# Kernel tuning notes

Measured on AMD Instinct MI355X. Metric: run time of the kernel, lower is better.

The kernel has to match this reference:

```python
import jax, jax.numpy as jnp
import numpy as np

EPS = 1e-5


def setup_inputs() -> dict:
    key = jax.random.key(0)
    ks = jax.random.split(key, 12)
    B, C, H, W = 1, 512, 64, 64
    d = C // 8
    inp = {
        "x": jax.random.normal(ks[0], (B, C, H, W), jnp.float32),
        "y": jax.random.normal(ks[1], (B, C, H, W), jnp.float32),
        "s_m": jax.random.uniform(ks[2], (H, W), jnp.float32),
        "q_m": jax.random.uniform(ks[3], (H, W), jnp.float32),
        "Wq": jax.random.normal(ks[4], (d, C), jnp.float32) * (1.0 / np.sqrt(C)),
        "bq": jnp.zeros((d,), jnp.float32),
        "Wk": jax.random.normal(ks[5], (d, C), jnp.float32) * (1.0 / np.sqrt(C)),
        "bk": jnp.zeros((d,), jnp.float32),
        "Wv": jax.random.normal(ks[6], (C, C), jnp.float32) * (1.0 / np.sqrt(C)),
        "bv": jnp.zeros((C,), jnp.float32),
        "W1": jax.random.normal(ks[7], (C, C), jnp.float32) * (1.0 / np.sqrt(C)),
        "b1": jnp.zeros((C,), jnp.float32),
        "W2": jax.random.normal(ks[8], (C, C), jnp.float32) * (1.0 / np.sqrt(C)),
        "b2": jnp.zeros((C,), jnp.float32),
        "gamma": jnp.ones((1, C, H, W), jnp.float32),
        "beta": jnp.zeros((1, C, H, W), jnp.float32),
    }
    return inp


def _conv1x1(x, Wt, b):
    # 1x1 Conv2d == per-pixel channel matmul
    return jnp.einsum("bchw,oc->bohw", x, Wt) + b[None, :, None, None]


def reference(x, y, s_m, q_m, Wq, bq, Wk, bk, Wv, bv, W1, b1, W2, b2, gamma, beta):
    B, C, H, W = x.shape
    N = H * W
    scale = (C // 8) ** (-0.5)

    q_m = jnp.where(q_m > 0.8, 1.0, 0.0).astype(x.dtype)
    x_fg = x * s_m[None, None]
    y_fg = y * q_m[None, None]

    def branch(q_in, k_in, v_in, use_max):
        q = _conv1x1(q_in, Wq, bq).reshape(B, -1, N).transpose(0, 2, 1) * scale  # [B,N,d]
        k = _conv1x1(k_in, Wk, bk).reshape(B, -1, N)                             # [B,d,N]
        v = _conv1x1(v_in, Wv, bv).reshape(B, -1, N)                             # [B,C,N]
        attn = jnp.einsum("bqd,bdk->bqk", q, k)                                  # [B,N,N]
        stat = jnp.max(attn) if use_max else jnp.min(attn)
        thr = (stat + jnp.mean(attn)) * 0.5
        attn = jnp.where(attn < thr, jnp.asarray(-999.0, attn.dtype), attn)
        attn = jax.nn.softmax(attn, axis=-1)
        out = jnp.einsum("bck,bqk->bcq", v, attn).reshape(B, C, H, W)
        h = out.transpose(0, 2, 3, 1)                                            # [B,H,W,C]
        h = jnp.maximum(h @ W1.T + b1, 0.0) @ W2.T + b2
        out = h.transpose(0, 3, 1, 2)
        # LayerNorm over all trailing dims [1,C,H,W] (B==1)
        mu = jnp.mean(out)
        var = jnp.mean((out - mu) ** 2)
        out = (out - mu) * jax.lax.rsqrt(var + EPS) * gamma + beta
        return out

    outx = branch(x_fg, y_fg, y_fg, True)
    outx = outx * s_m[None, None] + x * (1.0 - s_m)[None, None]
    outy = branch(y_fg, x, x, False)
    outy = outy * q_m[None, None] + y * (1.0 - q_m)[None, None]
    return outx, outy
```

## Files before the change

### kernel.cpp

```cpp
#include <hip/hip_runtime.h>
#include <math.h>

#define C_DIM 512
#define N_DIM 4096
#define CN (C_DIM * N_DIM)
#define SZO (N_DIM * C_DIM)
#define NN ((size_t)N_DIM * N_DIM)
#define NN_TOT ((long long)N_DIM * N_DIM)

typedef __attribute__((ext_vector_type(4))) float f32x4;
typedef __attribute__((ext_vector_type(8))) short short8;

__device__ __forceinline__ ushort f2bf(float f) {
    unsigned u = __float_as_uint(f);
    unsigned r = u + 0x7FFFu + ((u >> 16) & 1u);
    return (ushort)(r >> 16);
}
__device__ __forceinline__ float bf2f(ushort h) {
    return __uint_as_float((unsigned)h << 16);
}

__device__ __forceinline__ void gload16(const void* g, void* l) {
    __builtin_amdgcn_global_load_lds(
        (const __attribute__((address_space(1))) void*)g,
        (__attribute__((address_space(3))) void*)l, 16, 0, 0);
}

__global__ __launch_bounds__(256) void tconv64(
    const float* __restrict__ x, const float* __restrict__ y,
    ushort* __restrict__ xbT, ushort* __restrict__ ybT)
{
    const float* X = blockIdx.z ? y : x;
    ushort* XT = blockIdx.z ? ybT : xbT;
    __shared__ float t[64][65];
    const int c0 = blockIdx.x * 64;
    const int r0 = blockIdx.y * 64;
    const int ty = threadIdx.x >> 4, tx = threadIdx.x & 15;
    #pragma unroll
    for (int i = 0; i < 4; ++i) {
        int r = ty + i * 16;
        float4 v = *(const float4*)&X[(size_t)(r0 + r) * N_DIM + c0 + tx * 4];
        t[r][tx * 4 + 0] = v.x; t[r][tx * 4 + 1] = v.y;
        t[r][tx * 4 + 2] = v.z; t[r][tx * 4 + 3] = v.w;
    }
    __syncthreads();
    #pragma unroll
    for (int i = 0; i < 4; ++i) {
        int nn = ty + i * 16;
        ushort4 o;
        o.x = f2bf(t[tx * 4 + 0][nn]); o.y = f2bf(t[tx * 4 + 1][nn]);
        o.z = f2bf(t[tx * 4 + 2][nn]); o.w = f2bf(t[tx * 4 + 3][nn]);
        *(ushort4*)&XT[(size_t)(c0 + nn) * C_DIM + r0 + tx * 4] = o;
    }
}

__global__ __launch_bounds__(256) void cvtw3(
    const float* __restrict__ Wv, const float* __restrict__ W1,
    const float* __restrict__ W2, ushort* __restrict__ Wvb,
    ushort* __restrict__ W1b, ushort* __restrict__ W2b)
{
    const float* in  = (blockIdx.y == 0) ? Wv : (blockIdx.y == 1) ? W1 : W2;
    ushort*      out = (blockIdx.y == 0) ? Wvb : (blockIdx.y == 1) ? W1b : W2b;
    int i = (blockIdx.x * 256 + threadIdx.x) * 4;
    float4 v = *(const float4*)&in[i];
    ushort4 o = { f2bf(v.x), f2bf(v.y), f2bf(v.z), f2bf(v.w) };
    *(ushort4*)&out[i] = o;
}

template<int BM, int BN>
__global__ __launch_bounds__(256) void mfma_g(
    const ushort* __restrict__ A0, const ushort* __restrict__ A1,
    const ushort* __restrict__ B0, const ushort* __restrict__ B1,
    void* __restrict__ Out, size_t outBrStride,
    int M, int N, int K, int kLen, int nkz,
    const float* __restrict__ bias, int biasMode,
    const float* __restrict__ mask0, int mm0,
    const float* __restrict__ mask1, int mm1,
    int doRelu, int outBf16)
{
    constexpr int WAVES_M = BM / 64;
    constexpr int WAVES_N = 4 / WAVES_M;
    constexpr int WN = BN / WAVES_N;
    constexpr int FM = 4;
    constexpr int FN = WN / 16;
    constexpr int NCHUNK = (BM + BN) / 16;

    __shared__ ushort As[2][BM * 32];
    __shared__ ushort Bs[2][BN * 32];
    const int tid  = threadIdx.x;
    const int lane = tid & 63;
    const int wid  = tid >> 6;
    const int z  = blockIdx.z;
    const int br = z / nkz;
    const int kz = z % nkz;
    const ushort* A = br ? A1 : A0;
    const ushort* B = br ? B1 : B0;
    const float* mask = br ? mask1 : mask0;
    const int maskMode = br ? mm1 : mm0;

    const int m0 = blockIdx.y * BM, n0 = blockIdx.x * BN;
    const int wm = wid / WAVES_N, wn = wid % WAVES_N;
    const int wr = wm * 64, wc = wn * WN;
    const int kOff = kz * kLen;
    const int lrow = lane >> 2;
    const int lk   = (lane & 3) * 8;

    auto stage = [&](int buf, int t) {
        #pragma unroll
        for (int c = wid; c < NCHUNK; c += 4) {
            if (c < BM / 16) {
                gload16(A + (size_t)(m0 + c * 16 + lrow) * K + kOff + t * 32 + lk,
                        &As[buf][c * 512]);
            } else {
                int cb = c - BM / 16;
                gload16(B + (size_t)(n0 + cb * 16 + lrow) * K + kOff + t * 32 + lk,
                        &Bs[buf][cb * 512]);
            }
        }
    };

    f32x4 acc[FM][FN] = {};
    const int fr = lane & 15;
    const int k8 = (lane >> 4) * 8;
    const int nt = kLen / 32;

    stage(0, 0);
    asm volatile("s_waitcnt vmcnt(0)" ::: "memory");
    __syncthreads();
    int cur = 0;
    for (int t = 0; t < nt; ++t) {
        if (t + 1 < nt) stage(cur ^ 1, t + 1);
        short8 af[FM], bf[FN];
        #pragma unroll
        for (int mr = 0; mr < FM; ++mr)
            af[mr] = *(const short8*)&As[cur][(wr + mr * 16 + fr) * 32 + k8];
        #pragma unroll
        for (int nc = 0; nc < FN; ++nc)
            bf[nc] = *(const short8*)&Bs[cur][(wc + nc * 16 + fr) * 32 + k8];
        #pragma unroll
        for (int mr = 0; mr < FM; ++mr)
            #pragma unroll
            for (int nc = 0; nc < FN; ++nc)
                acc[mr][nc] = __builtin_amdgcn_mfma_f32_16x16x32_bf16(
                    af[mr], bf[nc], acc[mr][nc], 0, 0, 0);
        asm volatile("s_waitcnt vmcnt(0)" ::: "memory");
        __syncthreads();
        cur ^= 1;
    }

    const int orow = (lane >> 4) * 4;
    const int ocol = lane & 15;

    if (nkz > 1) {
        float* Of = (float*)Out + (size_t)z * M * N;
        #pragma unroll
        for (int mr = 0; mr < FM; ++mr)
            #pragma unroll
            for (int nc = 0; nc < FN; ++nc)
                #pragma unroll
                for (int j = 0; j < 4; ++j) {
                    int gm = m0 + wr + mr * 16 + orow + j;
                    int gn = n0 + wc + nc * 16 + ocol;
                    Of[(size_t)gm * N + gn] = acc[mr][nc][j];
                }
        return;
    }

    float mcol[FN], bcol[FN];
    #pragma unroll
    for (int nc = 0; nc < FN; ++nc) {
        int gn = n0 + wc + nc * 16 + ocol;
        mcol[nc] = (maskMode == 0) ? 1.0f
                 : (maskMode == 1) ? mask[gn]
                                   : (mask[gn] > 0.8f ? 1.0f : 0.0f);
        bcol[nc] = (biasMode == 2) ? bias[gn] : 0.0f;
    }
    ushort* Obf = (ushort*)Out + (size_t)br * outBrStride;
    float*  Of  = (float*)Out + (size_t)br * outBrStride;
    #pragma unroll
    for (int mr = 0; mr < FM; ++mr) {
        #pragma unroll
        for (int j = 0; j < 4; ++j) {
            int gm = m0 + wr + mr * 16 + orow + j;
            float brow = (biasMode == 1) ? bias[gm] : 0.0f;
            #pragma unroll
            for (int nc = 0; nc < FN; ++nc) {
                int gn = n0 + wc + nc * 16 + ocol;
                float v = acc[mr][nc][j] * mcol[nc] + brow + bcol[nc];
                if (doRelu) v = fmaxf(v, 0.0f);
                if (outBf16) Obf[(size_t)gm * N + gn] = f2bf(v);
                else         Of[(size_t)gm * N + gn] = v;
            }
        }
    }
}

__global__ __launch_bounds__(256) void qkraw(
    const float* __restrict__ Wq, const float* __restrict__ Wk,
    const float* __restrict__ x, const float* __restrict__ y,
    float* __restrict__ PX)
{
    const int mt   = blockIdx.y & 1;
    const int srcT = blockIdx.y >> 1;
    const int kz   = blockIdx.z;
    const float* W = mt ? Wk : Wq;
    const float* X = srcT ? y : x;

    __shared__ float As[16][65];
    __shared__ float Bs[16][65];
    const int tid = threadIdx.x;
    const int n0 = blockIdx.x * 64;
    const int ty = tid >> 4, tx = tid & 15;
    float acc[4][4] = {};
    const int kbase = kz * 128;

    for (int k0 = kbase; k0 < kbase + 128; k0 += 16) {
        {
            int mm = tid >> 2, kq = (tid & 3) * 4;
            const float4 w4 = *(const float4*)&W[(size_t)mm * 512 + k0 + kq];
            As[kq + 0][mm] = w4.x; As[kq + 1][mm] = w4.y;
            As[kq + 2][mm] = w4.z; As[kq + 3][mm] = w4.w;
        }
        {
            int kk = tid >> 4, nq = (tid & 15) * 4;
            *(float4*)&Bs[kk][nq] = *(const float4*)&X[(size_t)(k0 + kk) * N_DIM + n0 + nq];
        }
        __syncthreads();
        #pragma unroll
        for (int kk = 0; kk < 16; ++kk) {
            float a[4], b[4];
            #pragma unroll
            for (int r = 0; r < 4; ++r) a[r] = As[kk][ty * 4 + r];
            #pragma unroll
            for (int c = 0; c < 4; ++c) b[c] = Bs[kk][tx * 4 + c];
            #pragma unroll
            for (int r = 0; r < 4; ++r)
                #pragma unroll
                for (int c = 0; c < 4; ++c)
                    acc[r][c] = fmaf(a[r], b[c], acc[r][c]);
        }
        __syncthreads();
    }
    float* dst = PX + ((size_t)(kz * 2 + srcT) * 128 + mt * 64) * N_DIM;
    #pragma unroll
    for (int r = 0; r < 4; ++r) {
        float4 o = make_float4(acc[r][0], acc[r][1], acc[r][2], acc[r][3]);
        *(float4*)&dst[(size_t)(ty * 4 + r) * N_DIM + n0 + tx * 4] = o;
    }
}

__global__ __launch_bounds__(256) void qkfinish(
    const float* __restrict__ PX,
    const float* __restrict__ s_m, const float* __restrict__ q_m,
    const float* __restrict__ bq, const float* __restrict__ bk,
    ushort* __restrict__ QF0, ushort* __restrict__ KF0,
    ushort* __restrict__ QF1, ushort* __restrict__ KF1)
{
    int gid = blockIdx.x * 256 + threadIdx.x;
    int lane = gid & 63;
    int rest = gid >> 6;
    int blk = rest & 255;
    int tensor = rest >> 8;
    int fr = lane & 15, quad = lane >> 4;
    int n = blk * 16 + fr;

    int srcT, rowbase, isQ;
    const float* bias;
    ushort* dst;
    float mv, scale;
    if (tensor == 0)      { srcT = 0; rowbase = 0;  isQ = 1; bias = bq; dst = QF0; scale = 0.125f; mv = s_m[n]; }
    else if (tensor == 1) { srcT = 1; rowbase = 64; isQ = 0; bias = bk; dst = KF0; scale = 1.0f;   mv = (q_m[n] > 0.8f) ? 1.0f : 0.0f; }
    else if (tensor == 2) { srcT = 1; rowbase = 0;  isQ = 1; bias = bq; dst = QF1; scale = 0.125f; mv = (q_m[n] > 0.8f) ? 1.0f : 0.0f; }
    else                  { srcT = 0; rowbase = 64; isQ = 0; bias = bk; dst = KF1; scale = 1.0f;   mv = 1.0f; }

    ushort hi0[8], lo0[8], hi1[8], lo1[8];
    #pragma unroll
    for (int j = 0; j < 8; ++j) {
        int d0 = quad * 8 + j, d1 = 32 + d0;
        float v0 = 0.0f, v1 = 0.0f;
        #pragma unroll
        for (int kz = 0; kz < 4; ++kz) {
            size_t base = ((size_t)(kz * 2 + srcT) * 128 + rowbase);
            v0 += PX[(base + d0) * N_DIM + n];
            v1 += PX[(base + d1) * N_DIM + n];
        }
        v0 = (v0 * mv + bias[d0]) * scale;
        v1 = (v1 * mv + bias[d1]) * scale;
        hi0[j] = f2bf(v0); lo0[j] = f2bf(v0 - bf2f(hi0[j]));
        hi1[j] = f2bf(v1); lo1[j] = f2bf(v1 - bf2f(hi1[j]));
    }
    auto wr8 = [&](int kstep, const ushort* v) {
        size_t base = ((size_t)(blk * 6 + kstep) * 64 + lane) * 8;
        *(ushort4*)&dst[base]     = *(const ushort4*)&v[0];
        *(ushort4*)&dst[base + 4] = *(const ushort4*)&v[4];
    };
    wr8(0, hi0); wr8(1, hi1);
    if (isQ) { wr8(2, hi0); wr8(3, hi1); wr8(4, lo0); wr8(5, lo1); }
    else     { wr8(2, lo0); wr8(3, lo1); wr8(4, hi0); wr8(5, hi1); }
}

__device__ __forceinline__ void scores_mfma(
    const ushort* __restrict__ QF, const ushort* __restrict__ KF,
    int m0, int n0, int wr, int wc, int lane, f32x4 acc[4][4])
{
    const int blkA0 = (m0 + wr) >> 4;
    const int blkB0 = (n0 + wc) >> 4;
    #pragma unroll
    for (int s = 0; s < 6; ++s) {
        short8 af[4], bf[4];
        #pragma unroll
        for (int mr = 0; mr < 4; ++mr)
            af[mr] = *(const short8*)&QF[((size_t)((blkA0 + mr) * 6 + s) * 64 + lane) * 8];
        #pragma unroll
        for (int nc = 0; nc < 4; ++nc)
            bf[nc] = *(const short8*)&KF[((size_t)((blkB0 + nc) * 6 + s) * 64 + lane) * 8];
        #pragma unroll
        for (int mr = 0; mr < 4; ++mr)
            #pragma unroll
            for (int nc = 0; nc < 4; ++nc)
                acc[mr][nc] = __builtin_amdgcn_mfma_f32_16x16x32_bf16(
                    af[mr], bf[nc], acc[mr][nc], 0, 0, 0);
    }
}

__global__ __launch_bounds__(256) void scores_pass1(
    const ushort* __restrict__ QF0, const ushort* __restrict__ KF0,
    const ushort* __restrict__ QF1, const ushort* __restrict__ KF1,
    float* __restrict__ part, float* __restrict__ rowmaxp)
{
    const int br = blockIdx.z;
    const ushort* QF = br ? QF1 : QF0;
    const ushort* KF = br ? KF1 : KF0;
    part    += (size_t)br * 3072;
    rowmaxp += (size_t)br * 131072;

    const int lane = threadIdx.x & 63, wid = threadIdx.x >> 6;
    const int m0 = blockIdx.y * 128, n0 = blockIdx.x * 128;
    const int wr = (wid >> 1) * 64, wc = (wid & 1) * 64;
    f32x4 acc[4][4] = {};
    scores_mfma(QF, KF, m0, n0, wr, wc, lane, acc);

    float lmax = -3.4e38f, lmin = 3.4e38f, lsum = 0.0f;
    float rmx[4][4];
    #pragma unroll
    for (int mr = 0; mr < 4; ++mr)
        #pragma unroll
        for (int j = 0; j < 4; ++j) rmx[mr][j] = -3.4e38f;
    #pragma unroll
    for (int mr = 0; mr < 4; ++mr)
        #pragma unroll
        for (int nc = 0; nc < 4; ++nc)
            #pragma unroll
            for (int j = 0; j < 4; ++j) {
                float v = acc[mr][nc][j];
                lsum += v; lmax = fmaxf(lmax, v); lmin = fminf(lmin, v);
                rmx[mr][j] = fmaxf(rmx[mr][j], v);
            }
    #pragma unroll
    for (int m = 1; m < 16; m <<= 1)
        #pragma unroll
        for (int mr = 0; mr < 4; ++mr)
            #pragma unroll
            for (int j = 0; j < 4; ++j)
                rmx[mr][j] = fmaxf(rmx[mr][j], __shfl_xor(rmx[mr][j], m, 64));

    __shared__ float wrm[2][128];
    const int orow = (lane >> 4) * 4;
    if ((lane & 15) == 0) {
        #pragma unroll
        for (int mr = 0; mr < 4; ++mr)
            #pragma unroll
            for (int j = 0; j < 4; ++j)
                wrm[wid & 1][wr + mr * 16 + orow + j] = rmx[mr][j];
    }
    __syncthreads();
    if (threadIdx.x < 128) {
        float v = fmaxf(wrm[0][threadIdx.x], wrm[1][threadIdx.x]);
        rowmaxp[(size_t)blockIdx.x * 4096 + m0 + threadIdx.x] = v;
    }

    __shared__ float red[256];
    const int tid = threadIdx.x;
    const int bid = blockIdx.y * 32 + blockIdx.x;
    __syncthreads();
    red[tid] = lmax; __syncthreads();
    for (int s = 128; s > 0; s >>= 1) { if (tid < s) red[tid] = fmaxf(red[tid], red[tid + s]); __syncthreads(); }
    if (tid == 0) part[bid] = red[0];
    __syncthreads();
    red[tid] = lmin; __syncthreads();
    for (int s = 128; s > 0; s >>= 1) { if (tid < s) red[tid] = fminf(red[tid], red[tid + s]); __syncthreads(); }
    if (tid == 0) part[1024 + bid] = red[0];
    __syncthreads();
    red[tid] = lsum; __syncthreads();
    for (int s = 128; s > 0; s >>= 1) { if (tid < s) red[tid] += red[tid + s]; __syncthreads(); }
    if (tid == 0) part[2048 + bid] = red[0];
}

__global__ __launch_bounds__(256) void stats_fin2(
    const float* __restrict__ part, float* __restrict__ stats)
{
    const int br = blockIdx.x;
    part += (size_t)br * 3072;
    __shared__ float rmax[256], rmin[256];
    __shared__ double rsum[256];
    int tid = threadIdx.x;
    float m1 = -3.4e38f, m2 = 3.4e38f; double s = 0.0;
    for (int i = tid; i < 1024; i += 256) {
        m1 = fmaxf(m1, part[i]);
        m2 = fminf(m2, part[1024 + i]);
        s += (double)part[2048 + i];
    }
    rmax[tid] = m1; rmin[tid] = m2; rsum[tid] = s;
    __syncthreads();
    for (int st = 128; st > 0; st >>= 1) {
        if (tid < st) {
            rmax[tid] = fmaxf(rmax[tid], rmax[tid + st]);
            rmin[tid] = fminf(rmin[tid], rmin[tid + st]);
            rsum[tid] += rsum[tid + st];
        }
        __syncthreads();
    }
    if (tid == 0) {
        float stat = (br == 0) ? rmax[0] : rmin[0];
        float mean = (float)(rsum[0] / (double)NN_TOT);
        stats[br] = 0.5f * (stat + mean);
    }
}

__global__ __launch_bounds__(256) void row_fin(
    const float* __restrict__ rowmaxp, const float* __restrict__ stats,
    float* __restrict__ rowm)
{
    const int br = blockIdx.y;
    int r = blockIdx.x * 256 + threadIdx.x;
    float thr = stats[br];
    float m = -3.4e38f;
    #pragma unroll 8
    for (int b = 0; b < 32; ++b)
        m = fmaxf(m, rowmaxp[(size_t)br * 131072 + (size_t)b * 4096 + r]);
    rowm[br * 4096 + r] = (m >= thr) ? m : -1e30f;
}

__global__ __launch_bounds__(256) void scores_pass2(
    const ushort* __restrict__ QF0, const ushort* __restrict__ KF0,
    const ushort* __restrict__ QF1, const ushort* __restrict__ KF1,
    const float* __restrict__ stats, const float* __restrict__ rowm,
    ushort* __restrict__ Pe, float* __restrict__ rowsump)
{
    const int br = blockIdx.z;
    const ushort* QF = br ? QF1 : QF0;
    const ushort* KF = br ? KF1 : KF0;
    ushort* P = Pe + (size_t)br * NN;
    rowsump += (size_t)br * 131072;
    rowm    += (size_t)br * 4096;

    const int lane = threadIdx.x & 63, wid = threadIdx.x >> 6;
    const int m0 = blockIdx.y * 128, n0 = blockIdx.x * 128;
    const int wr = (wid >> 1) * 64, wc = (wid & 1) * 64;
    f32x4 acc[4][4] = {};
    scores_mfma(QF, KF, m0, n0, wr, wc, lane, acc);

    const float thr = stats[br];
    const int orow = (lane >> 4) * 4;
    const int ocol = lane & 15;
    float rm[4][4], rs[4][4];
    #pragma unroll
    for (int mr = 0; mr < 4; ++mr)
        #pragma unroll
        for (int j = 0; j < 4; ++j) {
            rm[mr][j] = rowm[m0 + wr + mr * 16 + orow + j];
            rs[mr][j] = 0.0f;
        }
    #pragma unroll
    for (int mr = 0; mr < 4; ++mr)
        #pragma unroll
        for (int nc = 0; nc < 4; ++nc)
            #pragma unroll
            for (int j = 0; j < 4; ++j) {
                float s = acc[mr][nc][j];
                float m = rm[mr][j];
                float e = (s < thr) ? 0.0f : __expf(s - m);
                if (m < -1e29f) e = 1.0f;
                ushort h = f2bf(e);
                rs[mr][j] += bf2f(h);
                P[(size_t)(m0 + wr + mr * 16 + orow + j) * N_DIM
                  + n0 + wc + nc * 16 + ocol] = h;
            }
    #pragma unroll
    for (int m = 1; m < 16; m <<= 1)
        #pragma unroll
        for (int mr = 0; mr < 4; ++mr)
            #pragma unroll
            for (int j = 0; j < 4; ++j)
                rs[mr][j] += __shfl_xor(rs[mr][j], m, 64);

    __shared__ float wrs[2][128];
    if ((lane & 15) == 0) {
        #pragma unroll
        for (int mr = 0; mr < 4; ++mr)
            #pragma unroll
            for (int j = 0; j < 4; ++j)
                wrs[wid & 1][wr + mr * 16 + orow + j] = rs[mr][j];
    }
    __syncthreads();
    if (threadIdx.x < 128)
        rowsump[(size_t)blockIdx.x * 4096 + m0 + threadIdx.x] =
            wrs[0][threadIdx.x] + wrs[1][threadIdx.x];
}

__global__ __launch_bounds__(256) void rsum_fin(
    const float* __restrict__ rowsump, float* __restrict__ invr)
{
    const int br = blockIdx.y;
    int r = blockIdx.x * 256 + threadIdx.x;
    float s = 0.0f;
    #pragma unroll 8
    for (int b = 0; b < 32; ++b)
        s += rowsump[(size_t)br * 131072 + (size_t)b * 4096 + r];
    invr[br * 4096 + r] = 1.0f / s;
}

__global__ __launch_bounds__(256) void reduce2row(
    const float* __restrict__ P4, const float* __restrict__ invr,
    ushort* __restrict__ O)
{
    const int br = blockIdx.y;
    int i = (blockIdx.x * 256 + threadIdx.x) * 4;
    int row = i >> 9;
    float sc = invr[br * 4096 + row];
    float4 a = *(const float4*)&P4[(size_t)(br * 2 + 0) * SZO + i];
    float4 b = *(const float4*)&P4[(size_t)(br * 2 + 1) * SZO + i];
    ushort4 o;
    o.x = f2bf((a.x + b.x) * sc);
    o.y = f2bf((a.y + b.y) * sc);
    o.z = f2bf((a.z + b.z) * sc);
    o.w = f2bf((a.w + b.w) * sc);
    *(ushort4*)&O[(size_t)br * SZO + i] = o;
}

__global__ __launch_bounds__(256) void ln_partial(
    const float* __restrict__ H2, float* __restrict__ lnp)
{
    const int br = blockIdx.y;
    const float* X = H2 + (size_t)br * CN;
    float* part = lnp + (size_t)br * 2048;
    __shared__ float rs[256], rq[256];
    int tid = threadIdx.x;
    size_t base = (size_t)blockIdx.x * 2048;
    float s = 0.0f, q = 0.0f;
    #pragma unroll
    for (int k = 0; k < 8; ++k) {
        float v = X[base + tid + k * 256];
        s += v; q = fmaf(v, v, q);
    }
    rs[tid] = s; rq[tid] = q; __syncthreads();
    for (int st = 128; st > 0; st >>= 1) {
        if (tid < st) { rs[tid] += rs[tid + st]; rq[tid] += rq[tid + st]; }
        __syncthreads();
    }
    if (tid == 0) { part[blockIdx.x] = rs[0]; part[1024 + blockIdx.x] = rq[0]; }
}

__global__ __launch_bounds__(256) void ln_fin(
    const float* __restrict__ lnp, float* __restrict__ stats)
{
    const int br = blockIdx.x;
    const float* part = lnp + (size_t)br * 2048;
    __shared__ double rs[256], rq[256];
    int tid = threadIdx.x;
    double s = 0.0, q = 0.0;
    for (int i = tid; i < 1024; i += 256) { s += part[i]; q += part[1024 + i]; }
    rs[tid] = s; rq[tid] = q; __syncthreads();
    for (int st = 128; st > 0; st >>= 1) {
        if (tid < st) { rs[tid] += rs[tid + st]; rq[tid] += rq[tid + st]; }
        __syncthreads();
    }
    if (tid == 0) {
        double mu = rs[0] / (double)CN;
        double var = rq[0] / (double)CN - mu * mu;
        stats[4 + 2 * br] = (float)mu;
        stats[5 + 2 * br] = (float)(1.0 / sqrt(var + 1e-5));
    }
}

__global__ __launch_bounds__(256) void gate_write(
    const float* __restrict__ H2, const float* __restrict__ stats,
    const float* __restrict__ gamma, const float* __restrict__ beta,
    const float* __restrict__ x, const float* __restrict__ y,
    const float* __restrict__ s_m, const float* __restrict__ q_m,
    float* __restrict__ out)
{
    const int br = blockIdx.y;
    size_t idx = (size_t)blockIdx.x * 256 + threadIdx.x;
    int n = (int)(idx & (N_DIM - 1));
    float mu = stats[4 + 2 * br], rstd = stats[5 + 2 * br];
    float normed = (H2[(size_t)br * CN + idx] - mu) * rstd * gamma[idx] + beta[idx];
    float mv = br ? ((q_m[n] > 0.8f) ? 1.0f : 0.0f) : s_m[n];
    const float* resid = br ? y : x;
    out[(size_t)br * CN + idx] = normed * mv + resid[idx] * (1.0f - mv);
}

extern "C" void kernel_launch(void* const* d_in, const int* in_sizes, int n_in,
                              void* d_out, int out_size, void* d_ws, size_t ws_size,
                              hipStream_t stream)
{
    const float* x     = (const float*)d_in[0];
    const float* y     = (const float*)d_in[1];
    const float* s_m   = (const float*)d_in[2];
    const float* q_m   = (const float*)d_in[3];
    const float* Wq    = (const float*)d_in[4];
    const float* bq    = (const float*)d_in[5];
    const float* Wk    = (const float*)d_in[6];
    const float* bk    = (const float*)d_in[7];
    const float* Wv    = (const float*)d_in[8];
    const float* bv    = (const float*)d_in[9];
    const float* W1    = (const float*)d_in[10];
    const float* b1    = (const float*)d_in[11];
    const float* W2    = (const float*)d_in[12];
    const float* b2    = (const float*)d_in[13];
    const float* gamma = (const float*)d_in[14];
    const float* beta  = (const float*)d_in[15];
    float* out = (float*)d_out;

    float* ws = (float*)d_ws;
    float*  R1    = ws;
    float*  PX    = R1;
    float*  P4    = R1;
    ushort* QF0   = (ushort*)(R1 + 4194304);
    ushort* KF0   = QF0 + 786432;
    ushort* QF1   = KF0 + 786432;
    ushort* KF1   = QF1 + 786432;
    float*  SMALL = R1 + 8388608;
    float*  PART  = SMALL;
    float*  RMAXP = PART + 6144;
    float*  RSUMP = RMAXP + 262144;
    float*  ROWM  = RSUMP + 262144;
    float*  INVR  = ROWM + 8192;
    float*  LNP   = INVR + 8192;
    float*  STATS = LNP + 4096;
    ushort* Wvb   = (ushort*)(STATS + 64);
    ushort* W1b   = Wvb + 262144;
    ushort* W2b   = W1b + 262144;
    ushort* Vb    = W2b + 262144;
    ushort* R2    = Vb + 4194304;
    ushort* xbT   = R2;
    ushort* ybT   = R2 + 2097152;
    ushort* Pe    = R2;
    ushort* O1T   = R2;
    ushort* H1T   = R2 + 4194304;
    float*  H2    = (float*)(R2 + 8388608);

    tconv64<<<dim3(64, 8, 2), 256, 0, stream>>>(x, y, xbT, ybT);
    cvtw3<<<dim3(256, 3), 256, 0, stream>>>(Wv, W1, W2, Wvb, W1b, W2b);

    qkraw<<<dim3(64, 4, 4), 256, 0, stream>>>(Wq, Wk, x, y, PX);
    qkfinish<<<256, 256, 0, stream>>>(PX, s_m, q_m, bq, bk, QF0, KF0, QF1, KF1);

    mfma_g<128, 128><<<dim3(32, 4, 2), 256, 0, stream>>>(
        Wvb, Wvb, ybT, xbT, Vb, (size_t)CN,
        512, 4096, 512, 512, 1, bv, 1, q_m, 2, nullptr, 0, 0, 1);

    scores_pass1<<<dim3(32, 32, 2), 256, 0, stream>>>(QF0, KF0, QF1, KF1, PART, RMAXP);
    stats_fin2<<<2, 256, 0, stream>>>(PART, STATS);
    row_fin<<<dim3(16, 2), 256, 0, stream>>>(RMAXP, STATS, ROWM);
    scores_pass2<<<dim3(32, 32, 2), 256, 0, stream>>>(QF0, KF0, QF1, KF1, STATS, ROWM, Pe, RSUMP);
    rsum_fin<<<dim3(16, 2), 256, 0, stream>>>(RSUMP, INVR);

    mfma_g<128, 128><<<dim3(4, 32, 4), 256, 0, stream>>>(
        Pe, Pe + NN, Vb, Vb + CN, P4, 0,
        4096, 512, 4096, 2048, 2, nullptr, 0, nullptr, 0, nullptr, 0, 0, 0);
    reduce2row<<<dim3(2048, 2), 256, 0, stream>>>(P4, INVR, O1T);

    mfma_g<128, 64><<<dim3(8, 32, 2), 256, 0, stream>>>(
        O1T, O1T + SZO, W1b, W1b, H1T, (size_t)SZO,
        4096, 512, 512, 512, 1, b1, 2, nullptr, 0, nullptr, 0, 1, 1);

    mfma_g<64, 128><<<dim3(32, 8, 2), 256, 0, stream>>>(
        W2b, W2b, H1T, H1T + SZO, H2, (size_t)CN,
        512, 4096, 512, 512, 1, b2, 1, nullptr, 0, nullptr, 0, 0, 0);

    ln_partial<<<dim3(1024, 2), 256, 0, stream>>>(H2, LNP);
    ln_fin<<<2, 256, 0, stream>>>(LNP, STATS);
    gate_write<<<dim3(8192, 2), 256, 0, stream>>>(
        H2, STATS, gamma, beta, x, y, s_m, q_m, out);
}
```

Before: 247.1 us.

## Swizzle GEMM LDS, fuse LayerNorm partials, reorder grids, vectorize gate write

Applies an XOR swizzle to the GEMM LDS tile layout to cut bank conflicts on the fragment reads. Adds an optional swapxy launch mode so consecutive blocks walk M first, which changes cache reuse for the PV and FFN1 GEMMs. Fuses the LayerNorm sum and sum-of-squares partials into the FFN2 GEMM epilogue, removing the separate ln_partial pass over H2. Also halves the qkraw K-split count and vectorizes gate_write to float4; the fused reduction adds a shared-memory tree reduction at the end of every block of that GEMM.

```diff
diff --git a/kernel.cpp b/kernel.cpp
--- a/kernel.cpp
+++ b/kernel.cpp
@@ -72,11 +72,11 @@
     const ushort* __restrict__ A0, const ushort* __restrict__ A1,
     const ushort* __restrict__ B0, const ushort* __restrict__ B1,
     void* __restrict__ Out, size_t outBrStride,
-    int M, int N, int K, int kLen, int nkz,
+    int M, int N, int K, int kLen, int nkz, int swapxy,
     const float* __restrict__ bias, int biasMode,
     const float* __restrict__ mask0, int mm0,
     const float* __restrict__ mask1, int mm1,
-    int doRelu, int outBf16)
+    int doRelu, int outBf16, float* __restrict__ lnp)
 {
     constexpr int WAVES_M = BM / 64;
     constexpr int WAVES_N = 4 / WAVES_M;
@@ -98,22 +98,28 @@
     const float* mask = br ? mask1 : mask0;
     const int maskMode = br ? mm1 : mm0;
 
-    const int m0 = blockIdx.y * BM, n0 = blockIdx.x * BN;
+    const int bxm = swapxy ? blockIdx.x : blockIdx.y;
+    const int bxn = swapxy ? blockIdx.y : blockIdx.x;
+    const int m0 = bxm * BM, n0 = bxn * BN;
     const int wm = wid / WAVES_N, wn = wid % WAVES_N;
     const int wr = wm * 64, wc = wn * WN;
     const int kOff = kz * kLen;
     const int lrow = lane >> 2;
-    const int lk   = (lane & 3) * 8;
+    const int kbl  = lane & 3;
 
     auto stage = [&](int buf, int t) {
         #pragma unroll
         for (int c = wid; c < NCHUNK; c += 4) {
             if (c < BM / 16) {
-                gload16(A + (size_t)(m0 + c * 16 + lrow) * K + kOff + t * 32 + lk,
+                int r = c * 16 + lrow;
+                int kb = kbl ^ ((r >> 1) & 3);
+                gload16(A + (size_t)(m0 + r) * K + kOff + t * 32 + kb * 8,
                         &As[buf][c * 512]);
             } else {
                 int cb = c - BM / 16;
-                gload16(B + (size_t)(n0 + cb * 16 + lrow) * K + kOff + t * 32 + lk,
+                int r = cb * 16 + lrow;
+                int kb = kbl ^ ((r >> 1) & 3);
+                gload16(B + (size_t)(n0 + r) * K + kOff + t * 32 + kb * 8,
                         &Bs[buf][cb * 512]);
             }
         }
@@ -121,7 +127,7 @@
 
     f32x4 acc[FM][FN] = {};
     const int fr = lane & 15;
-    const int k8 = (lane >> 4) * 8;
+    const int kq = lane >> 4;
     const int nt = kLen / 32;
 
     stage(0, 0);
@@ -132,11 +138,15 @@
         if (t + 1 < nt) stage(cur ^ 1, t + 1);
         short8 af[FM], bf[FN];
         #pragma unroll
-        for (int mr = 0; mr < FM; ++mr)
-            af[mr] = *(const short8*)&As[cur][(wr + mr * 16 + fr) * 32 + k8];
-        #pragma unroll
-        for (int nc = 0; nc < FN; ++nc)
-            bf[nc] = *(const short8*)&Bs[cur][(wc + nc * 16 + fr) * 32 + k8];
+        for (int mr = 0; mr < FM; ++mr) {
+            int rA = wr + mr * 16 + fr;
+            af[mr] = *(const short8*)&As[cur][rA * 32 + (kq ^ ((rA >> 1) & 3)) * 8];
+        }
+        #pragma unroll
+        for (int nc = 0; nc < FN; ++nc) {
+            int rB = wc + nc * 16 + fr;
+            bf[nc] = *(const short8*)&Bs[cur][rB * 32 + (kq ^ ((rB >> 1) & 3)) * 8];
+        }
         #pragma unroll
         for (int mr = 0; mr < FM; ++mr)
             #pragma unroll
@@ -177,6 +187,7 @@
     }
     ushort* Obf = (ushort*)Out + (size_t)br * outBrStride;
     float*  Of  = (float*)Out + (size_t)br * outBrStride;
+    float lsum = 0.0f, lsq = 0.0f;
     #pragma unroll
     for (int mr = 0; mr < FM; ++mr) {
         #pragma unroll
@@ -190,7 +201,22 @@
                 if (doRelu) v = fmaxf(v, 0.0f);
                 if (outBf16) Obf[(size_t)gm * N + gn] = f2bf(v);
                 else         Of[(size_t)gm * N + gn] = v;
+                lsum += v; lsq = fmaf(v, v, lsq);
             }
+        }
+    }
+    if (lnp) {
+        __shared__ float redS[256], redQ[256];
+        redS[tid] = lsum; redQ[tid] = lsq;
+        __syncthreads();
+        for (int s = 128; s > 0; s >>= 1) {
+            if (tid < s) { redS[tid] += redS[tid + s]; redQ[tid] += redQ[tid + s]; }
+            __syncthreads();
+        }
+        if (tid == 0) {
+            int fb = blockIdx.y * gridDim.x + blockIdx.x;
+            lnp[br * 512 + fb] = redS[0];
+            lnp[br * 512 + 256 + fb] = redQ[0];
         }
     }
 }
@@ -212,9 +238,9 @@
     const int n0 = blockIdx.x * 64;
     const int ty = tid >> 4, tx = tid & 15;
     float acc[4][4] = {};
-    const int kbase = kz * 128;
-
-    for (int k0 = kbase; k0 < kbase + 128; k0 += 16) {
+    const int kbase = kz * 256;
+
+    for (int k0 = kbase; k0 < kbase + 256; k0 += 16) {
         {
             int mm = tid >> 2, kq = (tid & 3) * 4;
             const float4 w4 = *(const float4*)&W[(size_t)mm * 512 + k0 + kq];
@@ -279,7 +305,7 @@
         int d0 = quad * 8 + j, d1 = 32 + d0;
         float v0 = 0.0f, v1 = 0.0f;
         #pragma unroll
-        for (int kz = 0; kz < 4; ++kz) {
+        for (int kz = 0; kz < 2; ++kz) {
             size_t base = ((size_t)(kz * 2 + srcT) * 128 + rowbase);
             v0 += PX[(base + d0) * N_DIM + n];
             v1 += PX[(base + d1) * N_DIM + n];
@@ -538,39 +564,16 @@
     *(ushort4*)&O[(size_t)br * SZO + i] = o;
 }
 
-__global__ __launch_bounds__(256) void ln_partial(
-    const float* __restrict__ H2, float* __restrict__ lnp)
-{
-    const int br = blockIdx.y;
-    const float* X = H2 + (size_t)br * CN;
-    float* part = lnp + (size_t)br * 2048;
-    __shared__ float rs[256], rq[256];
-    int tid = threadIdx.x;
-    size_t base = (size_t)blockIdx.x * 2048;
-    float s = 0.0f, q = 0.0f;
-    #pragma unroll
-    for (int k = 0; k < 8; ++k) {
-        float v = X[base + tid + k * 256];
-        s += v; q = fmaf(v, v, q);
-    }
-    rs[tid] = s; rq[tid] = q; __syncthreads();
-    for (int st = 128; st > 0; st >>= 1) {
-        if (tid < st) { rs[tid] += rs[tid + st]; rq[tid] += rq[tid + st]; }
-        __syncthreads();
-    }
-    if (tid == 0) { part[blockIdx.x] = rs[0]; part[1024 + blockIdx.x] = rq[0]; }
-}
-
 __global__ __launch_bounds__(256) void ln_fin(
     const float* __restrict__ lnp, float* __restrict__ stats)
 {
     const int br = blockIdx.x;
-    const float* part = lnp + (size_t)br * 2048;
+    const float* part = lnp + (size_t)br * 512;
     __shared__ double rs[256], rq[256];
     int tid = threadIdx.x;
-    double s = 0.0, q = 0.0;
-    for (int i = tid; i < 1024; i += 256) { s += part[i]; q += part[1024 + i]; }
-    rs[tid] = s; rq[tid] = q; __syncthreads();
+    rs[tid] = (double)part[tid];
+    rq[tid] = (double)part[256 + tid];
+    __syncthreads();
     for (int st = 128; st > 0; st >>= 1) {
         if (tid < st) { rs[tid] += rs[tid + st]; rq[tid] += rq[tid + st]; }
         __syncthreads();
@@ -591,13 +594,28 @@
     float* __restrict__ out)
 {
     const int br = blockIdx.y;
-    size_t idx = (size_t)blockIdx.x * 256 + threadIdx.x;
-    int n = (int)(idx & (N_DIM - 1));
+    size_t i = ((size_t)blockIdx.x * 256 + threadIdx.x) * 4;
+    int n = (int)(i & (N_DIM - 1));
     float mu = stats[4 + 2 * br], rstd = stats[5 + 2 * br];
-    float normed = (H2[(size_t)br * CN + idx] - mu) * rstd * gamma[idx] + beta[idx];
-    float mv = br ? ((q_m[n] > 0.8f) ? 1.0f : 0.0f) : s_m[n];
+    float4 h = *(const float4*)&H2[(size_t)br * CN + i];
+    float4 g = *(const float4*)&gamma[i];
+    float4 b = *(const float4*)&beta[i];
     const float* resid = br ? y : x;
-    out[(size_t)br * CN + idx] = normed * mv + resid[idx] * (1.0f - mv);
+    float4 r = *(const float4*)&resid[i];
+    float4 o;
+    float vals[4] = { h.x, h.y, h.z, h.w };
+    float gs[4] = { g.x, g.y, g.z, g.w };
+    float bs[4] = { b.x, b.y, b.z, b.w };
+    float rs[4] = { r.x, r.y, r.z, r.w };
+    float os[4];
+    #pragma unroll
+    for (int j = 0; j < 4; ++j) {
+        float mv = br ? ((q_m[n + j] > 0.8f) ? 1.0f : 0.0f) : s_m[n + j];
+        float normed = (vals[j] - mu) * rstd * gs[j] + bs[j];
+        os[j] = normed * mv + rs[j] * (1.0f - mv);
+    }
+    o.x = os[0]; o.y = os[1]; o.z = os[2]; o.w = os[3];
+    *(float4*)&out[(size_t)br * CN + i] = o;
 }
 
 extern "C" void kernel_launch(void* const* d_in, const int* in_sizes, int n_in,
@@ -637,7 +655,7 @@
     float*  ROWM  = RSUMP + 262144;
     float*  INVR  = ROWM + 8192;
     float*  LNP   = INVR + 8192;
-    float*  STATS = LNP + 4096;
+    float*  STATS = LNP + 1024;
     ushort* Wvb   = (ushort*)(STATS + 64);
     ushort* W1b   = Wvb + 262144;
     ushort* W2b   = W1b + 262144;
@@ -653,12 +671,12 @@
     tconv64<<<dim3(64, 8, 2), 256, 0, stream>>>(x, y, xbT, ybT);
     cvtw3<<<dim3(256, 3), 256, 0, stream>>>(Wv, W1, W2, Wvb, W1b, W2b);
 
-    qkraw<<<dim3(64, 4, 4), 256, 0, stream>>>(Wq, Wk, x, y, PX);
+    qkraw<<<dim3(64, 4, 2), 256, 0, stream>>>(Wq, Wk, x, y, PX);
     qkfinish<<<256, 256, 0, stream>>>(PX, s_m, q_m, bq, bk, QF0, KF0, QF1, KF1);
 
     mfma_g<128, 128><<<dim3(32, 4, 2), 256, 0, stream>>>(
         Wvb, Wvb, ybT, xbT, Vb, (size_t)CN,
-        512, 4096, 512, 512, 1, bv, 1, q_m, 2, nullptr, 0, 0, 1);
+        512, 4096, 512, 512, 1, 0, bv, 1, q_m, 2, nullptr, 0, 0, 1, nullptr);
 
     scores_pass1<<<dim3(32, 32, 2), 256, 0, stream>>>(QF0, KF0, QF1, KF1, PART, RMAXP);
     stats_fin2<<<2, 256, 0, stream>>>(PART, STATS);
@@ -666,21 +684,20 @@
     scores_pass2<<<dim3(32, 32, 2), 256, 0, stream>>>(QF0, KF0, QF1, KF1, STATS, ROWM, Pe, RSUMP);
     rsum_fin<<<dim3(16, 2), 256, 0, stream>>>(RSUMP, INVR);
 
-    mfma_g<128, 128><<<dim3(4, 32, 4), 256, 0, stream>>>(
+    mfma_g<128, 128><<<dim3(32, 4, 4), 256, 0, stream>>>(
         Pe, Pe + NN, Vb, Vb + CN, P4, 0,
-        4096, 512, 4096, 2048, 2, nullptr, 0, nullptr, 0, nullptr, 0, 0, 0);
+        4096, 512, 4096, 2048, 2, 1, nullptr, 0, nullptr, 0, nullptr, 0, 0, 0, nullptr);
     reduce2row<<<dim3(2048, 2), 256, 0, stream>>>(P4, INVR, O1T);
 
-    mfma_g<128, 64><<<dim3(8, 32, 2), 256, 0, stream>>>(
+    mfma_g<128, 64><<<dim3(32, 8, 2), 256, 0, stream>>>(
         O1T, O1T + SZO, W1b, W1b, H1T, (size_t)SZO,
-        4096, 512, 512, 512, 1, b1, 2, nullptr, 0, nullptr, 0, 1, 1);
+        4096, 512, 512, 512, 1, 1, b1, 2, nullptr, 0, nullptr, 0, 1, 1, nullptr);
 
     mfma_g<64, 128><<<dim3(32, 8, 2), 256, 0, stream>>>(
         W2b, W2b, H1T, H1T + SZO, H2, (size_t)CN,
-        512, 4096, 512, 512, 1, b2, 1, nullptr, 0, nullptr, 0, 0, 0);
-
-    ln_partial<<<dim3(1024, 2), 256, 0, stream>>>(H2, LNP);
+        512, 4096, 512, 512, 1, 0, b2, 1, nullptr, 0, nullptr, 0, 0, 0, LNP);
+
     ln_fin<<<2, 256, 0, stream>>>(LNP, STATS);
-    gate_write<<<dim3(8192, 2), 256, 0, stream>>>(
+    gate_write<<<dim3(2048, 2), 256, 0, stream>>>(
         H2, STATS, gamma, beta, x, y, s_m, q_m, out);
 }
```

Result: faster. 240.5 us (-2.6%).
